# Performance work log

Measured on AMD Instinct MI355X. Metric: run time of the kernel, lower is better.

The kernel has to match this reference:

```python
import jax, jax.numpy as jnp
import numpy as np


def setup_inputs() -> dict:
    P, M_DIM, R_DIM = 1024, 64, 64
    key = jax.random.key(0)
    k1, k2, k3, k4, k5 = jax.random.split(key, 5)
    hidden_state = jax.random.normal(k1, (P, M_DIM), dtype=jnp.float32)
    rela_state = jax.random.normal(k2, (P, P, R_DIM), dtype=jnp.float32)
    corr_index = jax.random.normal(k3, (P, P, 2), dtype=jnp.float32)
    nei_index = jax.random.randint(k4, (P, P), 0, 2, dtype=jnp.int32)
    # attention: Linear(2*m_dim + r_dim, 1), weight init N(0, 0.2), bias 0
    W = jax.random.normal(k5, (2 * M_DIM + R_DIM,), dtype=jnp.float32) * 0.2
    b = jnp.zeros((), dtype=jnp.float32)
    return {"hidden_state": hidden_state, "rela_state": rela_state,
            "corr_index": corr_index, "nei_index": nei_index, "W": W, "b": b}


def reference(hidden_state, rela_state, corr_index, nei_index, W, b):
    # hidden_state: [P, m], rela_state: [P, P, r], nei_index: [P, P]
    # corr_index is only used in the original for an emptiness check; unused here.
    P, m = hidden_state.shape
    r = rela_state.shape[-1]
    mask = nei_index > 0  # [P, P]; entry (i, j): j is a neighbor source for row i
    # Original concatenates (rela_t, hi_t, nei_inputs) where hi_t[i,j]=h[i],
    # nei_inputs[i,j]=h[j]; the 192->1 linear decomposes into three dots.
    Wr, Wi, Wj = W[:r], W[r:r + m], W[r + m:]
    scores = (jnp.einsum('ijr,r->ij', rela_state, Wr)
              + (hidden_state @ Wi)[:, None]
              + (hidden_state @ Wj)[None, :]
              + b)  # [P, P]
    # Scatter scores into a zero grid, replace remaining zeros with -1e-6,
    # softmax over neighbors (dim 1) -- faithful to the original's quirk that
    # non-neighbor slots participate in the softmax with logit -1e-6.
    Pos = jnp.where(mask, scores, jnp.float32(0.0))
    Pos = jnp.where(Pos == 0, jnp.float32(-1e-6), Pos)
    Pos = jax.nn.softmax(Pos, axis=1)
    # Weighted sum of neighbor hidden states; non-neighbor weights zeroed.
    attn = jnp.where(mask, Pos, jnp.float32(0.0))  # [P, P]
    H_sum = jnp.einsum('ij,jd->id', attn, hidden_state)  # [P, m]
    return H_sum
```

## Files before the change

kernel.cpp:

```cpp
#include <hip/hip_runtime.h>

#define PDIM 1024

__global__ __launch_bounds__(256) void precompute_hij(
    const float* __restrict__ hidden, const float* __restrict__ W,
    float* __restrict__ hij)
{
    int idx = blockIdx.x * 256 + threadIdx.x;
    int row = idx & (PDIM - 1);
    const float* w = W + 64 + ((idx >> 10) << 6);
    const float4* h4 = reinterpret_cast<const float4*>(hidden + (row << 6));
    const float4* w4 = reinterpret_cast<const float4*>(w);
    float acc = 0.f;
#pragma unroll
    for (int k = 0; k < 16; ++k) {
        float4 a = h4[k], b = w4[k];
        acc += a.x * b.x + a.y * b.y + a.z * b.z + a.w * b.w;
    }
    hij[idx] = acc;
}

__global__ __launch_bounds__(256) void social_row(
    const float* __restrict__ hidden,
    const float* __restrict__ rela,
    const int*   __restrict__ nei,
    const float* __restrict__ W,
    const float* __restrict__ bptr,
    const float* __restrict__ hij,
    float* __restrict__ out)
{
    __shared__ float s_pos[PDIM];
    __shared__ int   s_nei[PDIM];
    __shared__ float s_part[256];
    __shared__ float s_red[8];

    const int i    = blockIdx.x;
    const int tid  = threadIdx.x;
    const int lane = tid & 63;
    const int wave = tid >> 6;
    const int q    = lane & 15;
    const int sub  = lane >> 4;

    {
        const int4* nr = reinterpret_cast<const int4*>(nei + ((size_t)i << 10));
        reinterpret_cast<int4*>(s_nei)[tid] = nr[tid];
    }

    const float hib = hij[i] + bptr[0];
    const float* hj = hij + PDIM;
    const float4 wr = reinterpret_cast<const float4*>(W)[q];

    __syncthreads();

    {
        const int jofs = (wave << 2) + sub;
        const float* rp = rela + (((size_t)i << 10) + jofs) * 64 + (q << 2);
#pragma unroll 4
        for (int t = 0; t < 64; ++t) {
            float4 rv = *reinterpret_cast<const float4*>(rp + (size_t)t * (16 * 64));
            float part = rv.x * wr.x + rv.y * wr.y + rv.z * wr.z + rv.w * wr.w;
            part += __shfl_xor(part, 1);
            part += __shfl_xor(part, 2);
            part += __shfl_xor(part, 4);
            part += __shfl_xor(part, 8);
            if (q == 0) {
                int j = jofs + (t << 4);
                float score = part + hib + hj[j];
                float pos = (s_nei[j] > 0) ? score : 0.0f;
                if (pos == 0.0f) pos = -1e-6f;
                s_pos[j] = pos;
            }
        }
    }
    __syncthreads();

    float p0 = s_pos[tid];
    float p1 = s_pos[tid + 256];
    float p2 = s_pos[tid + 512];
    float p3 = s_pos[tid + 768];

    float m = fmaxf(fmaxf(p0, p1), fmaxf(p2, p3));
#pragma unroll
    for (int d = 1; d < 64; d <<= 1) m = fmaxf(m, __shfl_xor(m, d));
    if (lane == 0) s_red[wave] = m;
    __syncthreads();
    const float M = fmaxf(fmaxf(s_red[0], s_red[1]), fmaxf(s_red[2], s_red[3]));

    float e0 = __expf(p0 - M);
    float e1 = __expf(p1 - M);
    float e2 = __expf(p2 - M);
    float e3 = __expf(p3 - M);
    float s = e0 + e1 + e2 + e3;
#pragma unroll
    for (int d = 1; d < 64; d <<= 1) s += __shfl_xor(s, d);
    if (lane == 0) s_red[4 + wave] = s;
    __syncthreads();
    const float S = s_red[4] + s_red[5] + s_red[6] + s_red[7];
    const float inv = 1.0f / S;

    s_pos[tid]       = (s_nei[tid]       > 0) ? e0 * inv : 0.0f;
    s_pos[tid + 256] = (s_nei[tid + 256] > 0) ? e1 * inv : 0.0f;
    s_pos[tid + 512] = (s_nei[tid + 512] > 0) ? e2 * inv : 0.0f;
    s_pos[tid + 768] = (s_nei[tid + 768] > 0) ? e3 * inv : 0.0f;
    __syncthreads();

    {
        const float4* h4 = reinterpret_cast<const float4*>(hidden);
        const int jofs = (wave << 2) + sub;
        float4 acc = make_float4(0.f, 0.f, 0.f, 0.f);
#pragma unroll 4
        for (int t = 0; t < 64; ++t) {
            int j = jofs + (t << 4);
            float a = s_pos[j];
            float4 hv = h4[(j << 4) + q];
            acc.x += a * hv.x; acc.y += a * hv.y;
            acc.z += a * hv.z; acc.w += a * hv.w;
        }
        acc.x += __shfl_xor(acc.x, 16); acc.x += __shfl_xor(acc.x, 32);
        acc.y += __shfl_xor(acc.y, 16); acc.y += __shfl_xor(acc.y, 32);
        acc.z += __shfl_xor(acc.z, 16); acc.z += __shfl_xor(acc.z, 32);
        acc.w += __shfl_xor(acc.w, 16); acc.w += __shfl_xor(acc.w, 32);
        if (sub == 0)
            reinterpret_cast<float4*>(s_part)[(wave << 4) + q] = acc;
    }
    __syncthreads();
    if (tid < 64) {
        float r = s_part[tid] + s_part[64 + tid] + s_part[128 + tid] + s_part[192 + tid];
        out[((size_t)i << 6) + tid] = r;
    }
}

extern "C" void kernel_launch(void* const* d_in, const int* in_sizes, int n_in,
                              void* d_out, int out_size, void* d_ws, size_t ws_size,
                              hipStream_t stream)
{
    const float* hidden = (const float*)d_in[0];
    const float* rela   = (const float*)d_in[1];
    const int*   nei    = (const int*)d_in[3];
    const float* W      = (const float*)d_in[4];
    const float* bptr   = (const float*)d_in[5];

    float* hij = (float*)d_ws;

    precompute_hij<<<8, 256, 0, stream>>>(hidden, W, hij);
    social_row<<<PDIM, 256, 0, stream>>>(hidden, rela, nei, W, bptr, hij,
                                         (float*)d_out);
}
```

Baseline: 400.1 us.

## Skip rela loads for non-neighbor pairs, compute scores per-thread in registers

Each thread now owns four consecutive j columns, keeps the neighbor mask in registers, and reads the 64-float rela row only when the pair is a neighbor. Masked-out entries get logit -1e-6 directly, which matches the reference, so the 256MB rela stream is roughly halved for this input. The shuffle reduction and the shared-memory staging of scores and mask are removed. The cost is uncoalesced per-thread row reads (each lane reads its own 256B row) and divergence from the data-dependent branch.

```diff
diff --git a/kernel.cpp b/kernel.cpp
--- a/kernel.cpp
+++ b/kernel.cpp
@@ -30,7 +30,6 @@
     float* __restrict__ out)
 {
     __shared__ float s_pos[PDIM];
-    __shared__ int   s_nei[PDIM];
     __shared__ float s_part[256];
     __shared__ float s_red[8];
 
@@ -38,59 +37,48 @@
     const int tid  = threadIdx.x;
     const int lane = tid & 63;
     const int wave = tid >> 6;
-    const int q    = lane & 15;
-    const int sub  = lane >> 4;
 
-    {
-        const int4* nr = reinterpret_cast<const int4*>(nei + ((size_t)i << 10));
-        reinterpret_cast<int4*>(s_nei)[tid] = nr[tid];
-    }
+    const int4 nv = reinterpret_cast<const int4*>(nei + ((size_t)i << 10))[tid];
+    const int act[4] = { nv.x > 0, nv.y > 0, nv.z > 0, nv.w > 0 };
 
     const float hib = hij[i] + bptr[0];
     const float* hj = hij + PDIM;
-    const float4 wr = reinterpret_cast<const float4*>(W)[q];
 
-    __syncthreads();
+    float pos[4];
+#pragma unroll
+    for (int k = 0; k < 4; ++k) {
+        const int j = (tid << 2) + k;
+        float p = -1e-6f;
+        if (act[k]) {
+            const float4* rp = reinterpret_cast<const float4*>(
+                rela + ((((size_t)i << 10) + j) << 6));
+            float a0 = 0.f, a1 = 0.f, a2 = 0.f, a3 = 0.f;
+#pragma unroll
+            for (int c = 0; c < 16; c += 4) {
+                float4 r0 = rp[c], r1 = rp[c + 1], r2 = rp[c + 2], r3 = rp[c + 3];
+                a0 += r0.x * W[4*c+0]  + r0.y * W[4*c+1]  + r0.z * W[4*c+2]  + r0.w * W[4*c+3];
+                a1 += r1.x * W[4*c+4]  + r1.y * W[4*c+5]  + r1.z * W[4*c+6]  + r1.w * W[4*c+7];
+                a2 += r2.x * W[4*c+8]  + r2.y * W[4*c+9]  + r2.z * W[4*c+10] + r2.w * W[4*c+11];
+                a3 += r3.x * W[4*c+12] + r3.y * W[4*c+13] + r3.z * W[4*c+14] + r3.w * W[4*c+15];
+            }
+            float score = (a0 + a1) + (a2 + a3) + hib + hj[j];
+            p = (score == 0.0f) ? -1e-6f : score;
+        }
+        pos[k] = p;
+    }
 
-    {
-        const int jofs = (wave << 2) + sub;
-        const float* rp = rela + (((size_t)i << 10) + jofs) * 64 + (q << 2);
-#pragma unroll 4
-        for (int t = 0; t < 64; ++t) {
-            float4 rv = *reinterpret_cast<const float4*>(rp + (size_t)t * (16 * 64));
-            float part = rv.x * wr.x + rv.y * wr.y + rv.z * wr.z + rv.w * wr.w;
-            part += __shfl_xor(part, 1);
-            part += __shfl_xor(part, 2);
-            part += __shfl_xor(part, 4);
-            part += __shfl_xor(part, 8);
-            if (q == 0) {
-                int j = jofs + (t << 4);
-                float score = part + hib + hj[j];
-                float pos = (s_nei[j] > 0) ? score : 0.0f;
-                if (pos == 0.0f) pos = -1e-6f;
-                s_pos[j] = pos;
-            }
-        }
-    }
-    __syncthreads();
-
-    float p0 = s_pos[tid];
-    float p1 = s_pos[tid + 256];
-    float p2 = s_pos[tid + 512];
-    float p3 = s_pos[tid + 768];
-
-    float m = fmaxf(fmaxf(p0, p1), fmaxf(p2, p3));
+    float m = fmaxf(fmaxf(pos[0], pos[1]), fmaxf(pos[2], pos[3]));
 #pragma unroll
     for (int d = 1; d < 64; d <<= 1) m = fmaxf(m, __shfl_xor(m, d));
     if (lane == 0) s_red[wave] = m;
     __syncthreads();
     const float M = fmaxf(fmaxf(s_red[0], s_red[1]), fmaxf(s_red[2], s_red[3]));
 
-    float e0 = __expf(p0 - M);
-    float e1 = __expf(p1 - M);
-    float e2 = __expf(p2 - M);
-    float e3 = __expf(p3 - M);
-    float s = e0 + e1 + e2 + e3;
+    float e0 = __expf(pos[0] - M);
+    float e1 = __expf(pos[1] - M);
+    float e2 = __expf(pos[2] - M);
+    float e3 = __expf(pos[3] - M);
+    float s = (e0 + e1) + (e2 + e3);
 #pragma unroll
     for (int d = 1; d < 64; d <<= 1) s += __shfl_xor(s, d);
     if (lane == 0) s_red[4 + wave] = s;
@@ -98,13 +86,17 @@
     const float S = s_red[4] + s_red[5] + s_red[6] + s_red[7];
     const float inv = 1.0f / S;
 
-    s_pos[tid]       = (s_nei[tid]       > 0) ? e0 * inv : 0.0f;
-    s_pos[tid + 256] = (s_nei[tid + 256] > 0) ? e1 * inv : 0.0f;
-    s_pos[tid + 512] = (s_nei[tid + 512] > 0) ? e2 * inv : 0.0f;
-    s_pos[tid + 768] = (s_nei[tid + 768] > 0) ? e3 * inv : 0.0f;
+    float4 attn;
+    attn.x = act[0] ? e0 * inv : 0.0f;
+    attn.y = act[1] ? e1 * inv : 0.0f;
+    attn.z = act[2] ? e2 * inv : 0.0f;
+    attn.w = act[3] ? e3 * inv : 0.0f;
+    reinterpret_cast<float4*>(s_pos)[tid] = attn;
     __syncthreads();
 
     {
+        const int q   = lane & 15;
+        const int sub = lane >> 4;
         const float4* h4 = reinterpret_cast<const float4*>(hidden);
         const int jofs = (wave << 2) + sub;
         float4 acc = make_float4(0.f, 0.f, 0.f, 0.f);
```

New measurement: 353.5 us. 1.13x faster.
